# Optimization experiments

Measured on AMD Instinct MI355X. Metric: run time of the kernel, lower is better.

## Reference

```python
import jax, jax.numpy as jnp
import numpy as np

E, C, M, H, O = 8, 4096, 1024, 4096, 1024

def setup_inputs() -> dict:
    key = jax.random.key(0)
    k = jax.random.split(key, 5)
    # kaiming-uniform-ish scales (exact init distribution not needed for correctness baseline)
    s1 = 1.0 / np.sqrt(M)
    s2 = 1.0 / np.sqrt(H)
    return {
        'x': jax.random.normal(k[0], (E, C, M), dtype=jnp.float32),
        'fc1_w': jax.random.uniform(k[1], (E, H, M), minval=-s1, maxval=s1, dtype=jnp.float32),
        'fc1_b': jax.random.uniform(k[2], (E, H), minval=-s1, maxval=s1, dtype=jnp.float32),
        'fc2_w': jax.random.uniform(k[3], (E, H, O), minval=-s2, maxval=s2, dtype=jnp.float32),
        'fc2_b': jax.random.uniform(k[4], (E, O), minval=-s2, maxval=s2, dtype=jnp.float32),
    }

def reference(x, fc1_w, fc1_b, fc2_w, fc2_b):
    # y = relu(x @ fc1_w^T + b1) @ fc2_w + b2, batched over experts e
    h = jnp.einsum('ecm,ehm->ech', x, fc1_w) + fc1_b[:, None, :]
    h = jax.nn.relu(h)
    y = jnp.einsum('ech,eho->eco', h, fc2_w) + fc2_b[:, None, :]
    return y
```

## Files before the change

kernel.cpp:

```cpp
#include <hip/hip_runtime.h>


typedef __bf16 bf16x8 __attribute__((ext_vector_type(8)));
typedef float f32x4 __attribute__((ext_vector_type(4)));

__device__ __forceinline__ unsigned short f2bf(float f) {
  union { float f; unsigned int u; } v; v.f = f;
  unsigned int u = v.u;
  u += 0x7fffu + ((u >> 16) & 1u);
  return (unsigned short)(u >> 16);
}

#define GLD_LDS16(gptr, lptr)                                               \
  __builtin_amdgcn_global_load_lds(                                         \
      (const __attribute__((address_space(1))) void*)(gptr),                \
      (__attribute__((address_space(3))) void*)(lptr), 16, 0, 0)

__global__ void cvt_bf16_kernel(const float* __restrict__ in,
                                unsigned short* __restrict__ out, long n) {
  long i = ((long)blockIdx.x * blockDim.x + threadIdx.x) * 4;
  if (i >= n) return;
  const float4 v = *(const float4*)(in + i);
  ushort4 o;
  o.x = f2bf(v.x); o.y = f2bf(v.y); o.z = f2bf(v.z); o.w = f2bf(v.w);
  *(ushort4*)(out + i) = o;
}

__global__ void transpose_cvt_kernel(const float* __restrict__ in,
                                     unsigned short* __restrict__ out,
                                     int H, int O, long istride, long ostride) {
  __shared__ unsigned short tile[32][33];
  const float* inp = in + (long)blockIdx.z * istride;
  unsigned short* outp = out + (long)blockIdx.z * ostride;
  const int o0 = blockIdx.x * 32, h0 = blockIdx.y * 32;
  const int tx = threadIdx.x, ty = threadIdx.y;
#pragma unroll
  for (int r = ty; r < 32; r += 8)
    tile[r][tx] = f2bf(inp[(long)(h0 + r) * O + o0 + tx]);
  __syncthreads();
#pragma unroll
  for (int r = ty; r < 32; r += 8)
    outp[(long)(o0 + r) * H + h0 + tx] = tile[tx][r];
}

#define BM 256
#define BN 256
#define BK 64

template <int EPI>
__global__ __launch_bounds__(512, 2) void gemm_bt_kernel(
    const unsigned short* __restrict__ A, const unsigned short* __restrict__ B,
    const float* __restrict__ bias, void* __restrict__ Cout,
    int Nd, int Kd, long sA, long sB, long sBias, long sC) {
  __shared__ unsigned short As[2][BM * BK];
  __shared__ unsigned short Bs[2][BN * BK];

  const int nbx = gridDim.x;
  const int nbxy = nbx * gridDim.y;
  const int nwg = nbxy * gridDim.z;
  int gid = blockIdx.x + nbx * blockIdx.y + nbxy * blockIdx.z;
  gid = (gid & 7) * (nwg >> 3) + (gid >> 3);
  const int bz = gid / nbxy;
  const int rem = gid - bz * nbxy;
  const int by = rem / nbx;
  const int bx = rem - by * nbx;

  const unsigned short* Ae = A + (long)bz * sA;
  const unsigned short* Be = B + (long)bz * sB;
  const float* be = bias + (long)bz * sBias;

  const int tid = threadIdx.x;
  const int wave = tid >> 6;
  const int lane = tid & 63;
  const int wm = wave >> 2;
  const int wn = wave & 3;
  const int fr = lane & 15;
  const int quad = lane >> 4;
  const int fsw = fr & 7;

  const int blockM = by * BM;
  const int blockN = bx * BN;

  const int srow = tid >> 3;
  const int skc = ((tid & 7) ^ (srow & 7)) * 8;
  const unsigned short* gA = Ae + (long)(blockM + srow) * Kd + skc;
  const unsigned short* gB = Be + (long)(blockN + srow) * Kd + skc;

#define STAGE_A(buf, band, kt)                                              \
  GLD_LDS16(gA + (long)(band) * Kd + (kt) * BK,                             \
            &As[buf][(band) * BK + wave * 512])
#define STAGE_B(buf, band, kt)                                              \
  GLD_LDS16(gB + (long)(band) * Kd + (kt) * BK,                             \
            &Bs[buf][(band) * BK + wave * 512])
#define STAGE_A_MH0(buf, kt) { STAGE_A(buf, 0, kt);   STAGE_A(buf, 128, kt); }
#define STAGE_A_MH1(buf, kt) { STAGE_A(buf, 64, kt);  STAGE_A(buf, 192, kt); }
#define STAGE_B_ALL(buf, kt) { STAGE_B(buf, 0, kt);   STAGE_B(buf, 64, kt);  \
                               STAGE_B(buf, 128, kt); STAGE_B(buf, 192, kt); }

#define BAR __builtin_amdgcn_s_barrier()
#define VMCNT8 asm volatile("s_waitcnt vmcnt(8)" ::: "memory")

  f32x4 acc[8][4];
#pragma unroll
  for (int a = 0; a < 8; ++a)
#pragma unroll
    for (int b = 0; b < 4; ++b) acc[a][b] = (f32x4){0.f, 0.f, 0.f, 0.f};

  const int NT = Kd / BK;

  const int aBase = (wm * 128 + fr) * BK;
  const int bBase = (wn * 64 + fr) * BK;
  const int s0 = (quad ^ fsw) * 8;
  const int s1 = ((4 + quad) ^ fsw) * 8;

  bf16x8 af[4][2], bw[4][2];

#define READ_AH(bf, h)                                                      \
  {                                                                         \
    _Pragma("unroll")                                                       \
    for (int mi = 0; mi < 4; ++mi) {                                        \
      const unsigned short* _p =                                            \
          &As[bf][aBase + ((h) * 64 + mi * 16) * BK];                       \
      af[mi][0] = *(const bf16x8*)(_p + s0);                                \
      af[mi][1] = *(const bf16x8*)(_p + s1);                                \
    }                                                                       \
  }

#define READ_B(bf)                                                          \
  {                                                                         \
    _Pragma("unroll")                                                       \
    for (int ni = 0; ni < 4; ++ni) {                                        \
      const unsigned short* _p = &Bs[bf][bBase + ni * 16 * BK];             \
      bw[ni][0] = *(const bf16x8*)(_p + s0);                                \
      bw[ni][1] = *(const bf16x8*)(_p + s1);                                \
    }                                                                       \
  }

#define MFMA_HALF(h)                                                        \
  __builtin_amdgcn_s_setprio(1);                                            \
  _Pragma("unroll")                                                         \
  for (int kk = 0; kk < 2; ++kk)                                            \
    _Pragma("unroll")                                                       \
    for (int mi = 0; mi < 4; ++mi)                                          \
      _Pragma("unroll")                                                     \
      for (int ni = 0; ni < 4; ++ni)                                        \
        acc[(h) * 4 + mi][ni] = __builtin_amdgcn_mfma_f32_16x16x32_bf16(    \
            af[mi][kk], bw[ni][kk], acc[(h) * 4 + mi][ni], 0, 0, 0);        \
  __builtin_amdgcn_s_setprio(0);

  STAGE_B_ALL(0, 0);
  STAGE_A_MH0(0, 0);
  STAGE_A_MH1(0, 0);
  STAGE_B_ALL(1, 1);
  STAGE_A_MH0(1, 1);
  VMCNT8;
  BAR;

  for (int it = 0; it < NT / 2; ++it) {
    const int U = 2 * it;
    const int kW = (U + 2 < NT) ? U + 2 : NT - 1;
    const int kX = (U + 3 < NT) ? U + 3 : NT - 1;

    READ_B(0);
    READ_AH(0, 0);
    STAGE_A_MH1(1, U + 1);
    MFMA_HALF(0);
    VMCNT8;
    BAR;

    READ_AH(0, 1);
    STAGE_B_ALL(0, kW);
    STAGE_A_MH0(0, kW);
    MFMA_HALF(1);
    VMCNT8;
    BAR;

    READ_B(1);
    READ_AH(1, 0);
    STAGE_A_MH1(0, kW);
    MFMA_HALF(0);
    VMCNT8;
    BAR;

    READ_AH(1, 1);
    STAGE_B_ALL(1, kX);
    STAGE_A_MH0(1, kX);
    MFMA_HALF(1);
    VMCNT8;
    BAR;
  }

  float bv[4];
#pragma unroll
  for (int ni = 0; ni < 4; ++ni) bv[ni] = be[blockN + wn * 64 + ni * 16 + fr];

  if (EPI == 0) {
    unsigned short* Co = (unsigned short*)Cout + (long)bz * sC;
#pragma unroll
    for (int mi = 0; mi < 8; ++mi) {
      const int m = blockM + wm * 128 + mi * 16 + quad * 4;
#pragma unroll
      for (int r = 0; r < 4; ++r) {
        const long rowoff = (long)(m + r) * Nd;
#pragma unroll
        for (int ni = 0; ni < 4; ++ni) {
          float v = acc[mi][ni][r] + bv[ni];
          v = v > 0.f ? v : 0.f;
          Co[rowoff + blockN + wn * 64 + ni * 16 + fr] = f2bf(v);
        }
      }
    }
  } else {
    float* Co = (float*)Cout + (long)bz * sC;
#pragma unroll
    for (int mi = 0; mi < 8; ++mi) {
      const int m = blockM + wm * 128 + mi * 16 + quad * 4;
#pragma unroll
      for (int r = 0; r < 4; ++r) {
        const long rowoff = (long)(m + r) * Nd;
#pragma unroll
        for (int ni = 0; ni < 4; ++ni)
          Co[rowoff + blockN + wn * 64 + ni * 16 + fr] = acc[mi][ni][r] + bv[ni];
      }
    }
  }
}

extern "C" void kernel_launch(void* const* d_in, const int* in_sizes, int n_in,
                              void* d_out, int out_size, void* d_ws,
                              size_t ws_size, hipStream_t stream) {
  const float* x  = (const float*)d_in[0];
  const float* w1 = (const float*)d_in[1];
  const float* b1 = (const float*)d_in[2];
  const float* w2 = (const float*)d_in[3];
  const float* b2 = (const float*)d_in[4];
  float* out = (float*)d_out;

  const int E = 8, C = 4096, M = 1024, H = 4096, O = 1024;
  const long nx  = (long)C * M;
  const long nw1 = (long)H * M;
  const long nw2 = (long)O * H;
  const long nh  = (long)C * H;

  unsigned short* ws = (unsigned short*)d_ws;
  const size_t needBatch = (size_t)(E * (nx + nw1 + nw2 + nh)) * 2;

  if (ws_size >= needBatch) {
    unsigned short* xb  = ws;
    unsigned short* w1b = xb + E * nx;
    unsigned short* w2t = w1b + E * nw1;
    unsigned short* hb  = w2t + E * nw2;
    const long tx = E * nx, tw1 = E * nw1;
    cvt_bf16_kernel<<<tx / 1024, 256, 0, stream>>>(x, xb, tx);
    cvt_bf16_kernel<<<tw1 / 1024, 256, 0, stream>>>(w1, w1b, tw1);
    transpose_cvt_kernel<<<dim3(O / 32, H / 32, E), dim3(32, 8), 0, stream>>>(
        w2, w2t, H, O, (long)H * O, (long)O * H);
    gemm_bt_kernel<0><<<dim3(H / BN, C / BM, E), 512, 0, stream>>>(
        xb, w1b, b1, hb, H, M, nx, nw1, H, nh);
    gemm_bt_kernel<1><<<dim3(O / BN, C / BM, E), 512, 0, stream>>>(
        hb, w2t, b2, out, O, H, nh, nw2, O, (long)C * O);
  } else {
    unsigned short* xb  = ws;
    unsigned short* w1b = xb + nx;
    unsigned short* w2t = w1b + nw1;
    unsigned short* hb  = w2t + nw2;
    for (int e = 0; e < E; ++e) {
      cvt_bf16_kernel<<<nx / 1024, 256, 0, stream>>>(x + e * nx, xb, nx);
      cvt_bf16_kernel<<<nw1 / 1024, 256, 0, stream>>>(w1 + e * nw1, w1b, nw1);
      transpose_cvt_kernel<<<dim3(O / 32, H / 32, 1), dim3(32, 8), 0, stream>>>(
          w2 + e * nw2, w2t, H, O, 0, 0);
      gemm_bt_kernel<0><<<dim3(H / BN, C / BM, 1), 512, 0, stream>>>(
          xb, w1b, b1 + (long)e * H, hb, H, M, 0, 0, 0, 0);
      gemm_bt_kernel<1><<<dim3(O / BN, C / BM, 1), 512, 0, stream>>>(
          hb, w2t, b2 + (long)e * O, out + e * nx, O, H, 0, 0, 0, 0);
    }
  }
}
```

Before: 898.7 us.

## Double-buffer LDS fragments in registers to prefetch ahead of MFMA phases

Splits the A and B register fragments into ping-pong sets (P/Q), so LDS reads for the next half-tile are issued before the current MFMA batch runs, not right before it. The global-to-LDS staging schedule is reordered and the vmcnt waits are adjusted (vmcnt 2/6 instead of 8), with a full drain in the prologue. This is meant to hide LDS read latency behind the matrix cores. In exchange it doubles fragment register usage, which may lower occupancy or cause spills, and the tighter waits may stall on global loads.

```diff
diff --git a/kernel.cpp b/kernel.cpp
--- a/kernel.cpp
+++ b/kernel.cpp
@@ -98,7 +98,9 @@
                                STAGE_B(buf, 128, kt); STAGE_B(buf, 192, kt); }
 
 #define BAR __builtin_amdgcn_s_barrier()
-#define VMCNT8 asm volatile("s_waitcnt vmcnt(8)" ::: "memory")
+#define VMCNT0 asm volatile("s_waitcnt vmcnt(0)" ::: "memory")
+#define VMCNT2 asm volatile("s_waitcnt vmcnt(2)" ::: "memory")
+#define VMCNT6 asm volatile("s_waitcnt vmcnt(6)" ::: "memory")
 
   f32x4 acc[8][4];
 #pragma unroll
@@ -113,30 +115,30 @@
   const int s0 = (quad ^ fsw) * 8;
   const int s1 = ((4 + quad) ^ fsw) * 8;
 
-  bf16x8 af[4][2], bw[4][2];
-
-#define READ_AH(bf, h)                                                      \
+  bf16x8 afP[4][2], afQ[4][2], bwP[4][2], bwQ[4][2];
+
+#define READ_AH_TO(dst, bf, h)                                              \
   {                                                                         \
     _Pragma("unroll")                                                       \
     for (int mi = 0; mi < 4; ++mi) {                                        \
       const unsigned short* _p =                                            \
           &As[bf][aBase + ((h) * 64 + mi * 16) * BK];                       \
-      af[mi][0] = *(const bf16x8*)(_p + s0);                                \
-      af[mi][1] = *(const bf16x8*)(_p + s1);                                \
+      dst[mi][0] = *(const bf16x8*)(_p + s0);                               \
+      dst[mi][1] = *(const bf16x8*)(_p + s1);                               \
     }                                                                       \
   }
 
-#define READ_B(bf)                                                          \
+#define READ_B_TO(dst, bf)                                                  \
   {                                                                         \
     _Pragma("unroll")                                                       \
     for (int ni = 0; ni < 4; ++ni) {                                        \
       const unsigned short* _p = &Bs[bf][bBase + ni * 16 * BK];             \
-      bw[ni][0] = *(const bf16x8*)(_p + s0);                                \
-      bw[ni][1] = *(const bf16x8*)(_p + s1);                                \
+      dst[ni][0] = *(const bf16x8*)(_p + s0);                               \
+      dst[ni][1] = *(const bf16x8*)(_p + s1);                               \
     }                                                                       \
   }
 
-#define MFMA_HALF(h)                                                        \
+#define MFMA_HALF_FR(h, afx, bwx)                                           \
   __builtin_amdgcn_s_setprio(1);                                            \
   _Pragma("unroll")                                                         \
   for (int kk = 0; kk < 2; ++kk)                                            \
@@ -145,48 +147,50 @@
       _Pragma("unroll")                                                     \
       for (int ni = 0; ni < 4; ++ni)                                        \
         acc[(h) * 4 + mi][ni] = __builtin_amdgcn_mfma_f32_16x16x32_bf16(    \
-            af[mi][kk], bw[ni][kk], acc[(h) * 4 + mi][ni], 0, 0, 0);        \
+            afx[mi][kk], bwx[ni][kk], acc[(h) * 4 + mi][ni], 0, 0, 0);      \
   __builtin_amdgcn_s_setprio(0);
 
   STAGE_B_ALL(0, 0);
   STAGE_A_MH0(0, 0);
   STAGE_A_MH1(0, 0);
+  VMCNT0;
+  BAR;
+  READ_B_TO(bwP, 0);
+  READ_AH_TO(afP, 0, 0);
   STAGE_B_ALL(1, 1);
   STAGE_A_MH0(1, 1);
-  VMCNT8;
-  BAR;
 
   for (int it = 0; it < NT / 2; ++it) {
     const int U = 2 * it;
     const int kW = (U + 2 < NT) ? U + 2 : NT - 1;
     const int kX = (U + 3 < NT) ? U + 3 : NT - 1;
 
-    READ_B(0);
-    READ_AH(0, 0);
+    READ_AH_TO(afQ, 0, 1);
     STAGE_A_MH1(1, U + 1);
-    MFMA_HALF(0);
-    VMCNT8;
-    BAR;
-
-    READ_AH(0, 1);
+    MFMA_HALF_FR(0, afP, bwP);
+    VMCNT2;
+    BAR;
+
+    READ_B_TO(bwQ, 1);
+    READ_AH_TO(afP, 1, 0);
     STAGE_B_ALL(0, kW);
     STAGE_A_MH0(0, kW);
-    MFMA_HALF(1);
-    VMCNT8;
-    BAR;
-
-    READ_B(1);
-    READ_AH(1, 0);
+    MFMA_HALF_FR(1, afQ, bwP);
+    VMCNT6;
+    BAR;
+
+    READ_AH_TO(afQ, 1, 1);
     STAGE_A_MH1(0, kW);
-    MFMA_HALF(0);
-    VMCNT8;
-    BAR;
-
-    READ_AH(1, 1);
+    MFMA_HALF_FR(0, afP, bwQ);
+    VMCNT2;
+    BAR;
+
+    READ_B_TO(bwP, 0);
+    READ_AH_TO(afP, 0, 0);
     STAGE_B_ALL(1, kX);
     STAGE_A_MH0(1, kX);
-    MFMA_HALF(1);
-    VMCNT8;
+    MFMA_HALF_FR(1, afQ, bwQ);
+    VMCNT6;
     BAR;
   }
 
```

After: 2.500 ms. +178.1%, slower.
